# Performance work log

Hardware: AMD Instinct MI355X
Metric: run time of the kernel (lower is better)

## Reference

```python
import jax, jax.numpy as jnp
import numpy as np

D_MODEL, D_INNER, D_CONV, D_STATE, DT_RANK = 1024, 2048, 4, 16, 64
ALPHA, CHUNK = 0.1, 64


def setup_inputs() -> dict:
    key = jax.random.key(0)
    ks = jax.random.split(key, 10)
    B, T = 2, 2048
    s = lambda k, shape, scale: jax.random.normal(k, shape, jnp.float32) * scale
    return {
        "x": s(ks[0], (B, T, D_MODEL), 1.0),
        "norm1_w": jnp.ones((D_MODEL,), jnp.float32),
        "norm2_w": jnp.ones((D_MODEL,), jnp.float32),
        "in_proj_w": s(ks[1], (2 * D_INNER, D_MODEL), 0.02),
        "in_proj_b": jnp.zeros((2 * D_INNER,), jnp.float32),
        "conv_w": s(ks[2], (D_INNER, 1, D_CONV), 0.1),
        "conv_b": jnp.zeros((D_INNER,), jnp.float32),
        "x_proj_w": s(ks[3], (DT_RANK + 2 * D_STATE, D_INNER), 0.02),
        "dt_proj_w": s(ks[4], (D_INNER, DT_RANK), 0.02),
        "dt_proj_b": s(ks[5], (D_INNER,), 0.02),
        "A_log": jnp.log(jnp.broadcast_to(jnp.arange(1, D_STATE + 1, dtype=jnp.float32), (D_INNER, D_STATE))) + 0.0,
        "D_ssm": jnp.ones((D_INNER,), jnp.float32),
        "out_proj_w": s(ks[6], (D_MODEL, D_INNER), 0.02),
        "out_proj_b": jnp.zeros((D_MODEL,), jnp.float32),
        "proj_write_w": s(ks[7], (D_MODEL, D_MODEL), 0.02),
        "proj_read_w": s(ks[8], (D_MODEL, D_MODEL), 0.02),
        "decay": jnp.float32(4.6),
    }


def rmsnorm(x, w, eps=1e-5):
    return x * jax.lax.rsqrt(jnp.mean(x * x, axis=-1, keepdims=True) + eps) * w


def mamba_block(x, in_w, in_b, conv_w, conv_b, xp_w, dt_w, dt_b, A_log, D_ssm, out_w, out_b):
    # canonical (mamba-minimal) selective-SSM block
    B, T, _ = x.shape
    xz = x @ in_w.T + in_b                      # (B,T,2*d_inner)
    xm, res = jnp.split(xz, 2, axis=-1)
    # causal depthwise conv over time
    xc = jax.lax.conv_general_dilated(
        xm.transpose(0, 2, 1), conv_w, (1,), [(D_CONV - 1, 0)],
        dimension_numbers=("NCH", "OIH", "NCH"), feature_group_count=D_INNER)
    xm = jax.nn.silu(xc.transpose(0, 2, 1) + conv_b)
    x_dbl = xm @ xp_w.T                         # (B,T,dt_rank+2*d_state)
    delta = jax.nn.softplus(x_dbl[..., :DT_RANK] @ dt_w.T + dt_b)
    Bm = x_dbl[..., DT_RANK:DT_RANK + D_STATE]
    Cm = x_dbl[..., DT_RANK + D_STATE:]
    A = -jnp.exp(A_log)                          # (d_inner, d_state)

    def step(h, ins):
        d_t, B_t, C_t, u_t = ins                 # (B,di),(B,ds),(B,ds),(B,di)
        dA = jnp.exp(d_t[:, :, None] * A)
        h = h * dA + (d_t * u_t)[:, :, None] * B_t[:, None, :]
        y = jnp.einsum("bds,bs->bd", h, C_t)
        return h, y

    h0 = jnp.zeros((B, D_INNER, D_STATE), x.dtype)
    _, ys = jax.lax.scan(step, h0, (delta.transpose(1, 0, 2), Bm.transpose(1, 0, 2),
                                    Cm.transpose(1, 0, 2), xm.transpose(1, 0, 2)))
    y = ys.transpose(1, 0, 2) + xm * D_ssm
    y = y * jax.nn.silu(res)
    return y @ out_w.T + out_b


def memory_attend(out, w_write, w_read, decay):
    # chunked Hebbian write/read (RetNet-style chunked linear attention)
    B, T, D = out.shape
    C = CHUNK
    gamma = jax.nn.sigmoid(decay)
    log_gamma = jnp.log(gamma)
    v = out @ w_write.T
    wk = jnp.pad(out[:, :-1], ((0, 0), (1, 0), (0, 0)))
    rk = out
    n = T // C
    p = jnp.arange(C)
    diffs = jnp.clip(p[:, None] - 1 - p[None, :], 0, None).astype(out.dtype)
    causal = (p[:, None] > p[None, :]).astype(out.dtype)
    M = jnp.exp(diffs * log_gamma) * causal      # (C,C) intra-chunk decay mask
    g_in = gamma ** p                            # (C,)
    g_w = gamma ** (C - 1 - p)                   # (C,)

    chunked = lambda a: a.reshape(B, n, C, D).transpose(1, 0, 2, 3)  # (n,B,C,D)

    def step(W, ins):
        rk_c, wk_c, v_c = ins                    # each (B,C,D)
        inter = jnp.einsum("bde,bce->bcd", W, rk_c) * g_in[None, :, None]
        S = jnp.einsum("bcd,bkd->bck", rk_c, wk_c)
        intra = jnp.einsum("bck,bkd->bcd", S * M, v_c)
        W_new = (gamma ** C) * W + jnp.einsum("bcd,bce->bde", v_c * g_w[None, :, None], wk_c)
        return W_new, inter + intra

    W0 = jnp.zeros((B, D, D), out.dtype)
    _, reads = jax.lax.scan(step, W0, (chunked(rk), chunked(wk), chunked(v)))
    reads = reads.transpose(1, 0, 2, 3).reshape(B, T, D)
    return out + ALPHA * (reads @ w_read.T)


def reference(x, norm1_w, norm2_w, in_proj_w, in_proj_b, conv_w, conv_b, x_proj_w,
              dt_proj_w, dt_proj_b, A_log, D_ssm, out_proj_w, out_proj_b,
              proj_write_w, proj_read_w, decay):
    mb = lambda h: mamba_block(h, in_proj_w, in_proj_b, conv_w, conv_b, x_proj_w,
                               dt_proj_w, dt_proj_b, A_log, D_ssm, out_proj_w, out_proj_b)
    out1 = mb(rmsnorm(x, norm1_w))
    x1 = x + out1
    out2 = mb(rmsnorm(x1, norm2_w))   # tied weights: same params as mamba1
    out2 = memory_attend(out2, proj_write_w, proj_read_w, decay)
    return x1 + out2
```

## Files before the change

### kernel.cpp

```cpp
#include <hip/hip_runtime.h>
#include <hip/hip_bf16.h>
#include <math.h>

typedef __hip_bfloat16 bf16;
typedef __attribute__((ext_vector_type(4))) float f32x4;
typedef __attribute__((ext_vector_type(8))) short bf16x8;
typedef __attribute__((ext_vector_type(8))) unsigned short u16x8;

static __device__ __forceinline__ float b2f(bf16 v) { return __bfloat162float(v); }
static __device__ __forceinline__ float us2f(unsigned short u) {
  union { unsigned short s; bf16 h; } c; c.s = u; return __bfloat162float(c.h);
}
static __device__ __forceinline__ void  stv(float* p, float v) { *p = v; }
static __device__ __forceinline__ void  stv(bf16* p, float v) { *p = __float2bfloat16(v); }
static __device__ __forceinline__ float ldin(const void* p, size_t i, int f) {
  return f ? ((const float*)p)[i] : b2f(((const bf16*)p)[i]);
}
static __device__ __forceinline__ unsigned short f2b(float x) {
  bf16 h = __float2bfloat16(x);
  return *reinterpret_cast<unsigned short*>(&h);
}

static __device__ __forceinline__ void gl16(const unsigned short* g,
                                            void* ldsbase, int byteoff) {
  __builtin_amdgcn_global_load_lds(
      (const __attribute__((address_space(1))) unsigned int*)g,
      (__attribute__((address_space(3))) unsigned int*)((char*)ldsbase + byteoff),
      16, 0, 0);
}

constexpr int B_  = 2;
constexpr int T_  = 2048;
constexpr int DM  = 1024;
constexpr int DI  = 2048;
constexpr int DS  = 16;
constexpr int DTR = 64;
constexpr int ROWS = B_ * T_;
constexpr int SL  = 32;
constexpr int NSC = T_ / SL;
constexpr int KSP = 4;

__global__ void detect_k(const void* __restrict__ decay, int* __restrict__ flag) {
  flag[0] = (((const unsigned short*)decay)[0] == 0x4093) ? 0 : 1;
  flag[1] = 0;
}

__global__ void sentinel_k(void* __restrict__ out, float val, int n,
                           const int* __restrict__ df) {
  int f = *df;
  int i = blockIdx.x * 256 + threadIdx.x;
  if (i < n) {
    if (f) ((float*)out)[i] = val;
    else   ((bf16*)out)[i] = __float2bfloat16(val);
  }
}

__global__ void cvt1_k(const void* __restrict__ src, bf16* __restrict__ dst, int n,
                       const int* __restrict__ df) {
  int f = *df;
  int i = blockIdx.x * 256 + threadIdx.x;
  if (i < n) stv(&dst[i], ldin(src, i, f));
}

__global__ void rmsnorm_k(const void* __restrict__ xin, const void* __restrict__ w,
                          bf16* __restrict__ out, const int* __restrict__ df,
                          int xin_raw) {
  int f = *df;
  int fx = xin_raw ? f : 0;
  int row = blockIdx.x;
  int tid = threadIdx.x;
  float ss = 0.f;
  for (int d = tid; d < DM; d += 256) {
    float v = ldin(xin, (size_t)row * DM + d, fx);
    ss += v * v;
  }
  for (int o = 32; o > 0; o >>= 1) ss += __shfl_down(ss, o, 64);
  __shared__ float sred[4];
  int lane = tid & 63, wid = tid >> 6;
  if (lane == 0) sred[wid] = ss;
  __syncthreads();
  if (tid == 0) {
    float t = sred[0] + sred[1] + sred[2] + sred[3];
    sred[0] = 1.f / sqrtf(t / DM + 1e-5f);
  }
  __syncthreads();
  float rs = sred[0];
  for (int d = tid; d < DM; d += 256) {
    float v = ldin(xin, (size_t)row * DM + d, fx);
    stv(&out[(size_t)row * DM + d], v * rs * ldin(w, d, f));
  }
}

__global__ void transpose_k(const bf16* __restrict__ src, bf16* __restrict__ dst) {
  __shared__ unsigned short tile[64][65];
  int b = blockIdx.z;
  int t0 = blockIdx.x * 64, d0 = blockIdx.y * 64;
  int tid = threadIdx.x;
  int lt = tid & 63, lq = tid >> 6;
  const unsigned short* sp = (const unsigned short*)src;
  unsigned short* dp = (unsigned short*)dst;
#pragma unroll
  for (int i = 0; i < 16; i++) {
    int r = lq * 16 + i;
    tile[r][lt] = sp[((size_t)b * T_ + t0 + r) * DM + d0 + lt];
  }
  __syncthreads();
#pragma unroll
  for (int i = 0; i < 16; i++) {
    int r = lq * 16 + i;
    dp[((size_t)b * DM + d0 + r) * T_ + t0 + lt] = tile[lt][r];
  }
}

__global__ __launch_bounds__(512, 2)
void gemm256_k(const bf16* __restrict__ A, int lda,
               const void* __restrict__ B, int ldb,
               const void* __restrict__ bias,
               bf16* __restrict__ C, int ldc, int K,
               const int* __restrict__ df) {
  __shared__ alignas(16) unsigned char smem[65536];
  int f = *df;
  int m0 = blockIdx.y * 256, n0 = blockIdx.x * 256;
  int tid = threadIdx.x;
  int wave = tid >> 6, lane = tid & 63, quad = lane >> 4, l15 = lane & 15;
  int wrow = wave >> 2, wcol = wave & 3;
  const unsigned short* Ag = (const unsigned short*)A;
  const unsigned short* Bg = (const unsigned short*)B;
  f32x4 acc[8][4] = {};

  int r0 = tid >> 2;
  int kc = (((tid & 3) ^ ((r0 >> 1) & 3))) * 8;
  int xq = (quad ^ ((l15 >> 1) & 3)) * 16;

  auto stg = [&](int t, int isB, int dd) {
    const unsigned short* src = isB ? Bg : Ag;
    int ld = isB ? ldb : lda;
    int x0 = isB ? n0 : m0;
    int rbase = (isB ? 32768 : 0) + dd * 16384;
    int kk = t * 32;
    gl16(src + (size_t)(x0 + r0) * ld + kk + kc, smem, rbase + wave * 1024);
    gl16(src + (size_t)(x0 + r0 + 128) * ld + kk + kc, smem,
         rbase + 8192 + wave * 1024);
  };
  auto rdA = [&](int dd, int fr) {
    return *(const bf16x8*)(smem + dd * 16384 + wrow * 8192 + fr * 1024 +
                            l15 * 64 + xq);
  };
  auto rdB = [&](int dd, int fc) {
    return *(const bf16x8*)(smem + 32768 + dd * 16384 + wcol * 4096 +
                            fc * 1024 + l15 * 64 + xq);
  };

  int NT = K >> 5;
  if (f) {
    for (int t = 0; t < NT; ++t) {
      stg(t, 0, 0);
      {
        int r = tid >> 1, h = (tid & 1) * 16;
        const float* bp = (const float*)B + (size_t)(n0 + r) * ldb + t * 32 + h;
        float4 x0 = *(const float4*)bp,       x1 = *(const float4*)(bp + 4);
        float4 x2 = *(const float4*)(bp + 8), x3 = *(const float4*)(bp + 12);
        union { unsigned short s[8]; uint4 v; } p0, p1;
        p0.s[0]=f2b(x0.x); p0.s[1]=f2b(x0.y); p0.s[2]=f2b(x0.z); p0.s[3]=f2b(x0.w);
        p0.s[4]=f2b(x1.x); p0.s[5]=f2b(x1.y); p0.s[6]=f2b(x1.z); p0.s[7]=f2b(x1.w);
        p1.s[0]=f2b(x2.x); p1.s[1]=f2b(x2.y); p1.s[2]=f2b(x2.z); p1.s[3]=f2b(x2.w);
        p1.s[4]=f2b(x3.x); p1.s[5]=f2b(x3.y); p1.s[6]=f2b(x3.z); p1.s[7]=f2b(x3.w);
        int rx = (r >> 1) & 3;
        int c0 = (tid & 1) * 2;
        *(uint4*)(smem + 32768 + r * 64 + ((c0 ^ rx) * 16))       = p0.v;
        *(uint4*)(smem + 32768 + r * 64 + (((c0 + 1) ^ rx) * 16)) = p1.v;
      }
      __syncthreads();
      bf16x8 af[8], bv0, bv1, bv2, bv3;
#pragma unroll
      for (int fr = 0; fr < 8; fr++) af[fr] = rdA(0, fr);
      bv0 = rdB(0, 0); bv1 = rdB(0, 1); bv2 = rdB(0, 2); bv3 = rdB(0, 3);
#pragma unroll
      for (int fr = 0; fr < 8; fr++) {
        acc[fr][0] = __builtin_amdgcn_mfma_f32_16x16x32_bf16(af[fr], bv0, acc[fr][0], 0, 0, 0);
        acc[fr][1] = __builtin_amdgcn_mfma_f32_16x16x32_bf16(af[fr], bv1, acc[fr][1], 0, 0, 0);
        acc[fr][2] = __builtin_amdgcn_mfma_f32_16x16x32_bf16(af[fr], bv2, acc[fr][2], 0, 0, 0);
        acc[fr][3] = __builtin_amdgcn_mfma_f32_16x16x32_bf16(af[fr], bv3, acc[fr][3], 0, 0, 0);
      }
      __syncthreads();
    }
  } else {
    stg(0, 0, 0); stg(0, 1, 0);
    stg(1, 0, 1);
    asm volatile("s_waitcnt vmcnt(2)" ::: "memory");
    __builtin_amdgcn_sched_barrier(0);
    __builtin_amdgcn_s_barrier();
    for (int t = 0; t < NT; ++t) {
      int d = t & 1;
      bf16x8 af[8], bv0, bv1;
#pragma unroll
      for (int fr = 0; fr < 8; fr++) af[fr] = rdA(d, fr);
      bv0 = rdB(d, 0); bv1 = rdB(d, 1);
      if (t + 1 < NT) stg(t + 1, 1, d ^ 1);
      __builtin_amdgcn_s_barrier();
      asm volatile("s_waitcnt lgkmcnt(0)" ::: "memory");
      __builtin_amdgcn_sched_barrier(0);
      __builtin_amdgcn_s_setprio(1);
#pragma unroll
      for (int fr = 0; fr < 8; fr++) {
        acc[fr][0] = __builtin_amdgcn_mfma_f32_16x16x32_bf16(af[fr], bv0, acc[fr][0], 0, 0, 0);
        acc[fr][1] = __builtin_amdgcn_mfma_f32_16x16x32_bf16(af[fr], bv1, acc[fr][1], 0, 0, 0);
      }
      __builtin_amdgcn_s_setprio(0);
      __builtin_amdgcn_s_barrier();
      bf16x8 bv2, bv3;
      bv2 = rdB(d, 2); bv3 = rdB(d, 3);
      if (t + 2 < NT) stg(t + 2, 0, d);
      __builtin_amdgcn_s_barrier();
      asm volatile("s_waitcnt lgkmcnt(0)" ::: "memory");
      __builtin_amdgcn_sched_barrier(0);
      __builtin_amdgcn_s_setprio(1);
#pragma unroll
      for (int fr = 0; fr < 8; fr++) {
        acc[fr][2] = __builtin_amdgcn_mfma_f32_16x16x32_bf16(af[fr], bv2, acc[fr][2], 0, 0, 0);
        acc[fr][3] = __builtin_amdgcn_mfma_f32_16x16x32_bf16(af[fr], bv3, acc[fr][3], 0, 0, 0);
      }
      __builtin_amdgcn_s_setprio(0);
      if (t + 1 < NT) {
        if (t + 2 < NT)
          asm volatile("s_waitcnt vmcnt(2)" ::: "memory");
        else
          asm volatile("s_waitcnt vmcnt(0)" ::: "memory");
        __builtin_amdgcn_sched_barrier(0);
        __builtin_amdgcn_s_barrier();
      }
    }
  }

#pragma unroll
  for (int fr = 0; fr < 8; fr++) {
#pragma unroll
    for (int rr = 0; rr < 4; rr++) {
      int row = m0 + wrow * 128 + fr * 16 + quad * 4 + rr;
#pragma unroll
      for (int fc = 0; fc < 4; fc++) {
        int col = n0 + wcol * 64 + fc * 16 + l15;
        float v = acc[fr][fc][rr];
        if (bias) v += ldin(bias, col, f);
        C[(size_t)row * ldc + col] = __float2bfloat16(v);
      }
    }
  }
}

template <int MODE, int ACT, int MROWS>
__global__ void mgemm_k(const bf16* __restrict__ A, size_t sAz, int lda,
                        const void* __restrict__ B, size_t sBz, int ldb,
                        const void* __restrict__ bias,
                        bf16* __restrict__ C, size_t sCz, int ldc,
                        int M, int N, int K,
                        const void* __restrict__ dec, const int* __restrict__ df) {
  constexpr int FR = MROWS / 32;
  int by = (MODE == 2) ? ((int)gridDim.y - 1 - (int)blockIdx.y) : (int)blockIdx.y;
  int m0 = by * MROWS, n0 = blockIdx.x * 128;
  if (MODE == 1 && n0 > m0 + MROWS - 1) return;
  int f = *df;
  int bz = blockIdx.z;
  const bf16* Ab = A + (size_t)bz * sAz;
  const unsigned short* Bb16 =
      (const unsigned short*)B + (size_t)bz * sBz;
  bf16* Cb = C + (size_t)bz * sCz;
  int kmax = (MODE == 2) ? (m0 + MROWS) : K;
  __shared__ alignas(16) unsigned short As[2][MROWS][32];
  __shared__ alignas(16) unsigned short Bs[2][128][32];
  int tid = threadIdx.x;
  int wave = tid >> 6, lane = tid & 63, quad = lane >> 4, l15 = lane & 15;
  int wr = (wave >> 1) * (MROWS / 2), wc = (wave & 1) * 64;
  f32x4 acc[FR][4] = {};
  int lrow = lane >> 2;
  int lh = (((lane & 3) ^ ((lrow >> 1) & 3))) * 8;
  int xqs = (quad ^ ((l15 >> 1) & 3)) * 8;
  const unsigned short* Aus = (const unsigned short*)Ab;

  auto stage = [&](int buf, int k0) {
    if (MROWS == 128) {
#pragma unroll
      for (int q = 0; q < 2; q++) {
        int seg = wave * 2 + q;
        int rowa = seg * 16 + lrow;
        gl16(Aus + (size_t)(m0 + rowa) * lda + k0 + lh, &As[buf][0][0],
             seg * 1024);
      }
    } else {
      int rowa = wave * 16 + lrow;
      gl16(Aus + (size_t)(m0 + rowa) * lda + k0 + lh, &As[buf][0][0],
           wave * 1024);
    }
    if (MODE == 0 && f) {
      int r = tid >> 1, h = (tid & 1) * 16;
      const float* bp = (const float*)B + (size_t)(n0 + r) * ldb + k0 + h;
      float4 x0 = *(const float4*)bp,       x1 = *(const float4*)(bp + 4);
      float4 x2 = *(const float4*)(bp + 8), x3 = *(const float4*)(bp + 12);
      union { unsigned short s[8]; uint4 v; } p0, p1;
      p0.s[0]=f2b(x0.x); p0.s[1]=f2b(x0.y); p0.s[2]=f2b(x0.z); p0.s[3]=f2b(x0.w);
      p0.s[4]=f2b(x1.x); p0.s[5]=f2b(x1.y); p0.s[6]=f2b(x1.z); p0.s[7]=f2b(x1.w);
      p1.s[0]=f2b(x2.x); p1.s[1]=f2b(x2.y); p1.s[2]=f2b(x2.z); p1.s[3]=f2b(x2.w);
      p1.s[4]=f2b(x3.x); p1.s[5]=f2b(x3.y); p1.s[6]=f2b(x3.z); p1.s[7]=f2b(x3.w);
      int rx = (r >> 1) & 3;
      int c0 = (tid & 1) * 2;
      *(uint4*)&Bs[buf][r][(c0 ^ rx) * 8]       = p0.v;
      *(uint4*)&Bs[buf][r][((c0 + 1) ^ rx) * 8] = p1.v;
    } else {
#pragma unroll
      for (int q = 0; q < 2; q++) {
        int seg = wave * 2 + q;
        int rowb = seg * 16 + lrow;
        gl16(Bb16 + (size_t)(n0 + rowb) * ldb + k0 + lh, &Bs[buf][0][0],
             seg * 1024);
      }
    }
  };

  auto compute = [&](int buf) {
    bf16x8 af[FR], bfv[4];
#pragma unroll
    for (int i = 0; i < FR; i++)
      af[i] = *(const bf16x8*)&As[buf][wr + 16 * i + l15][xqs];
#pragma unroll
    for (int j = 0; j < 4; j++)
      bfv[j] = *(const bf16x8*)&Bs[buf][wc + 16 * j + l15][xqs];
#pragma unroll
    for (int i = 0; i < FR; i++)
#pragma unroll
      for (int j = 0; j < 4; j++)
        acc[i][j] = __builtin_amdgcn_mfma_f32_16x16x32_bf16(af[i], bfv[j],
                                                            acc[i][j], 0, 0, 0);
  };

  int nt = kmax >> 5;
  stage(0, 0);
  __syncthreads();
  int cur = 0;
  for (int t = 0; t < nt - 1; ++t) {
    stage(cur ^ 1, (t + 1) * 32);
    compute(cur);
    __syncthreads();
    cur ^= 1;
  }
  compute(cur);

  float lg = 0.f;
  if (MODE == 1) {
    float g = 1.f / (1.f + __expf(-ldin(dec, 0, f)));
    lg = __logf(g);
  }
#pragma unroll
  for (int i = 0; i < FR; i++) {
#pragma unroll
    for (int rr = 0; rr < 4; rr++) {
      int row = m0 + wr + 16 * i + quad * 4 + rr;
      if (MODE == 1 && n0 == 0 && wc == 0 && l15 == 0)
        Cb[(size_t)row * ldc] = __float2bfloat16(0.f);
#pragma unroll
      for (int j = 0; j < 4; j++) {
        int col = n0 + wc + 16 * j + l15;
        float v = acc[i][j][rr];
        if (MODE == 0) {
          if (bias) v += ldin(bias, col, f);
          if (ACT == 1) v = (v > 20.f) ? v : log1pf(__expf(v));
          Cb[(size_t)row * ldc + col] = __float2bfloat16(v);
        } else if (MODE == 1) {
          int colp = col + 1;
          int d_ = row - colp;
          v = (d_ > 0) ? v * __expf(lg * (float)(d_ - 1)) : 0.f;
          if (colp < N)
            Cb[(size_t)row * ldc + colp] = __float2bfloat16(v);
        } else {
          Cb[(size_t)row * ldc + col] = __float2bfloat16(v);
        }
      }
    }
  }
}

__global__ void conv_silu_k(const bf16* __restrict__ xz, const void* __restrict__ cw,
                            const void* __restrict__ cb, bf16* __restrict__ xm,
                            const int* __restrict__ df) {
  int f = *df;
  int i = blockIdx.x * 256 + threadIdx.x;
  int d8 = i & (DI / 8 - 1);
  int t = (i >> 8) & (T_ - 1);
  int b = i >> 19;
  int d0 = d8 * 8;
  const unsigned short* xzu =
      (const unsigned short*)xz + (size_t)b * T_ * 2 * DI + d0;

  float w[8][4], bias8[8];
  if (f) {
    const float* cwf = (const float*)cw + (size_t)d0 * 4;
#pragma unroll
    for (int j = 0; j < 8; j++) {
      float4 q = *(const float4*)(cwf + j * 4);
      w[j][0] = q.x; w[j][1] = q.y; w[j][2] = q.z; w[j][3] = q.w;
    }
    float4 b0 = *(const float4*)((const float*)cb + d0);
    float4 b1 = *(const float4*)((const float*)cb + d0 + 4);
    bias8[0] = b0.x; bias8[1] = b0.y; bias8[2] = b0.z; bias8[3] = b0.w;
    bias8[4] = b1.x; bias8[5] = b1.y; bias8[6] = b1.z; bias8[7] = b1.w;
  } else {
    const unsigned short* cwu = (const unsigned short*)cw + (size_t)d0 * 4;
#pragma unroll
    for (int jj = 0; jj < 4; jj++) {
      u16x8 q = *(const u16x8*)(cwu + jj * 8);
#pragma unroll
      for (int e = 0; e < 8; e++)
        w[(jj * 8 + e) >> 2][(jj * 8 + e) & 3] = us2f(q[e]);
    }
    u16x8 bb = *(const u16x8*)((const unsigned short*)cb + d0);
#pragma unroll
    for (int j = 0; j < 8; j++) bias8[j] = us2f(bb[j]);
  }

  float s[8];
#pragma unroll
  for (int j = 0; j < 8; j++) s[j] = bias8[j];

  if (t >= 3) {
    u16x8 v0 = *(const u16x8*)(xzu + (size_t)(t - 3) * 2 * DI);
    u16x8 v1 = *(const u16x8*)(xzu + (size_t)(t - 2) * 2 * DI);
    u16x8 v2 = *(const u16x8*)(xzu + (size_t)(t - 1) * 2 * DI);
    u16x8 v3 = *(const u16x8*)(xzu + (size_t)t * 2 * DI);
#pragma unroll
    for (int j = 0; j < 8; j++)
      s[j] += w[j][0] * us2f(v0[j]) + w[j][1] * us2f(v1[j]) +
              w[j][2] * us2f(v2[j]) + w[j][3] * us2f(v3[j]);
  } else {
#pragma unroll
    for (int k = 0; k < 4; k++) {
      int tt = t - 3 + k;
      if (tt >= 0) {
        u16x8 v = *(const u16x8*)(xzu + (size_t)tt * 2 * DI);
#pragma unroll
        for (int j = 0; j < 8; j++) s[j] += w[j][k] * us2f(v[j]);
      }
    }
  }
  union { unsigned short us[8]; u16x8 v; } o;
#pragma unroll
  for (int j = 0; j < 8; j++)
    o.us[j] = f2b(s[j] / (1.f + __expf(-s[j])));
  *(u16x8*)((unsigned short*)xm + (size_t)i * 8) = o.v;
}

__global__ void xproj_k(const bf16* __restrict__ xm, const void* __restrict__ xpw,
                        bf16* __restrict__ parts, const int* __restrict__ df) {
  int f = *df;
  int m0 = blockIdx.x * 128;
  int z = blockIdx.y;
  int kbase = z * (DI / KSP);
  __shared__ alignas(16) unsigned short As[2][128][32];
  __shared__ alignas(16) unsigned short Bs[2][96][32];
  int tid = threadIdx.x;
  int wave = tid >> 6, lane = tid & 63, quad = lane >> 4, l15 = lane & 15;
  int wr = wave * 32;
  f32x4 acc[2][6] = {};
  int lrow = lane >> 2;
  int lh = (((lane & 3) ^ ((lrow >> 1) & 3))) * 8;
  int xqs = (quad ^ ((l15 >> 1) & 3)) * 8;
  const unsigned short* Aus = (const unsigned short*)xm;
  const unsigned short* Bus = (const unsigned short*)xpw;

  auto stage = [&](int buf, int k0) {
#pragma unroll
    for (int q = 0; q < 2; q++) {
      int seg = wave * 2 + q;
      int rowa = seg * 16 + lrow;
      gl16(Aus + (size_t)(m0 + rowa) * DI + kbase + k0 + lh, &As[buf][0][0],
           seg * 1024);
    }
    if (f) {
      if (tid < 192) {
        int r2 = tid >> 1, h2 = (tid & 1) * 16;
        const float* bp = (const float*)xpw + (size_t)r2 * DI + kbase + k0 + h2;
        float4 x0 = *(const float4*)bp,       x1 = *(const float4*)(bp + 4);
        float4 x2 = *(const float4*)(bp + 8), x3 = *(const float4*)(bp + 12);
        union { unsigned short s[8]; uint4 v; } p0, p1;
        p0.s[0]=f2b(x0.x); p0.s[1]=f2b(x0.y); p0.s[2]=f2b(x0.z); p0.s[3]=f2b(x0.w);
        p0.s[4]=f2b(x1.x); p0.s[5]=f2b(x1.y); p0.s[6]=f2b(x1.z); p0.s[7]=f2b(x1.w);
        p1.s[0]=f2b(x2.x); p1.s[1]=f2b(x2.y); p1.s[2]=f2b(x2.z); p1.s[3]=f2b(x2.w);
        p1.s[4]=f2b(x3.x); p1.s[5]=f2b(x3.y); p1.s[6]=f2b(x3.z); p1.s[7]=f2b(x3.w);
        int rx = (r2 >> 1) & 3;
        int c0 = (tid & 1) * 2;
        *(uint4*)&Bs[buf][r2][(c0 ^ rx) * 8]       = p0.v;
        *(uint4*)&Bs[buf][r2][((c0 + 1) ^ rx) * 8] = p1.v;
      }
    } else if (wave < 3) {
#pragma unroll
      for (int q = 0; q < 2; q++) {
        int seg = wave * 2 + q;
        int rowb = seg * 16 + lrow;
        gl16(Bus + (size_t)rowb * DI + kbase + k0 + lh, &Bs[buf][0][0],
             seg * 1024);
      }
    }
  };

  auto compute = [&](int buf) {
    bf16x8 af[2], bfv[6];
#pragma unroll
    for (int i = 0; i < 2; i++)
      af[i] = *(const bf16x8*)&As[buf][wr + 16 * i + l15][xqs];
#pragma unroll
    for (int j = 0; j < 6; j++)
      bfv[j] = *(const bf16x8*)&Bs[buf][16 * j + l15][xqs];
#pragma unroll
    for (int i = 0; i < 2; i++)
#pragma unroll
      for (int j = 0; j < 6; j++)
        acc[i][j] = __builtin_amdgcn_mfma_f32_16x16x32_bf16(af[i], bfv[j],
                                                            acc[i][j], 0, 0, 0);
  };

  constexpr int NT = (DI / KSP) / 32;
  stage(0, 0);
  __syncthreads();
  int cur = 0;
  for (int t = 0; t < NT - 1; ++t) {
    stage(cur ^ 1, (t + 1) * 32);
    compute(cur);
    __syncthreads();
    cur ^= 1;
  }
  compute(cur);

  bf16* out = parts + (size_t)z * ROWS * 96;
#pragma unroll
  for (int i = 0; i < 2; i++)
#pragma unroll
    for (int rr = 0; rr < 4; rr++) {
      int row = m0 + wr + 16 * i + quad * 4 + rr;
#pragma unroll
      for (int j = 0; j < 6; j++) {
        int col = 16 * j + l15;
        out[(size_t)row * 96 + col] = __float2bfloat16(acc[i][j][rr]);
      }
    }
}

__global__ void reduce_xdbl_k(const bf16* __restrict__ parts, bf16* __restrict__ xdbl) {
  int i = blockIdx.x * 256 + threadIdx.x;
  if (i >= ROWS * 96) return;
  float s = 0.f;
#pragma unroll
  for (int z = 0; z < KSP; z++) s += b2f(parts[(size_t)z * ROWS * 96 + i]);
  stv(&xdbl[i], s);
}

__global__ void scan_p1_k(const bf16* __restrict__ delta, const bf16* __restrict__ xm,
                          const bf16* __restrict__ xdbl,
                          const void* __restrict__ alog,
                          bf16* __restrict__ F, float* __restrict__ S,
                          const int* __restrict__ df) {
  int f = *df;
  int idx = blockIdx.x * 256 + threadIdx.x;
  int d = idx & (DI - 1);
  int c = (idx >> 11) & (NSC - 1);
  int b = idx >> 17;
  float A[DS], hh[DS];
  bool fastA = true;
#pragma unroll
  for (int s = 0; s < DS; s++) {
    A[s] = -__expf(ldin(alog, d * DS + s, f));
    fastA = fastA && (fabsf(A[s] + (float)(s + 1)) < 1e-3f);
    hh[s] = 0.f;
  }
  int cs = c * SL;
  float ssum = 0.f;
  if (fastA) {
    for (int t = cs; t < cs + SL; t++) {
      size_t r = (size_t)b * T_ + t;
      float dlt = b2f(delta[r * DI + d]);
      float u = b2f(xm[r * DI + d]);
      ssum += dlt;
      float du = dlt * u;
      float q = __expf(-dlt);
      u16x8 t0 = *(const u16x8*)(xdbl + r * 96 + 64);
      u16x8 t1 = *(const u16x8*)(xdbl + r * 96 + 72);
      float e = 1.f;
#pragma unroll
      for (int s = 0; s < 8; s++) {
        e *= q; hh[s] = hh[s] * e + du * us2f(t0[s]);
      }
#pragma unroll
      for (int s = 0; s < 8; s++) {
        e *= q; hh[8 + s] = hh[8 + s] * e + du * us2f(t1[s]);
      }
    }
  } else {
    for (int t = cs; t < cs + SL; t++) {
      size_t r = (size_t)b * T_ + t;
      float dlt = b2f(delta[r * DI + d]);
      float u = b2f(xm[r * DI + d]);
      ssum += dlt;
      float du = dlt * u;
      u16x8 t0 = *(const u16x8*)(xdbl + r * 96 + 64);
      u16x8 t1 = *(const u16x8*)(xdbl + r * 96 + 72);
#pragma unroll
      for (int s = 0; s < 8; s++) {
        hh[s]     = hh[s]     * __expf(dlt * A[s])     + du * us2f(t0[s]);
        hh[8 + s] = hh[8 + s] * __expf(dlt * A[8 + s]) + du * us2f(t1[s]);
      }
    }
  }
#pragma unroll
  for (int s = 0; s < DS; s++) stv(&F[(size_t)idx * 16 + s], hh[s]);
  S[idx] = ssum;
}

__global__ void scan_p2_k(bf16* __restrict__ F, const float* __restrict__ S,
                          const void* __restrict__ alog, const int* __restrict__ df) {
  int f = *df;
  int idx = blockIdx.x * 256 + threadIdx.x;
  int s = idx & 15;
  int d = (idx >> 4) & (DI - 1);
  int b = idx >> 15;
  float As_ = -__expf(ldin(alog, d * DS + s, f));
  float H = 0.f;
  for (int c = 0; c < NSC; c++) {
    size_t base = (size_t)(b * NSC + c) * DI + d;
    float tmp = b2f(F[base * 16 + s]);
    stv(&F[base * 16 + s], H);
    H = __expf(As_ * S[base]) * H + tmp;
  }
}

__global__ void scan_p3_k(bf16* __restrict__ delta, const bf16* __restrict__ xm,
                          const bf16* __restrict__ xz, const bf16* __restrict__ xdbl,
                          const void* __restrict__ alog, const void* __restrict__ dssm,
                          const bf16* __restrict__ F, const int* __restrict__ df) {
  int f = *df;
  int idx = blockIdx.x * 256 + threadIdx.x;
  int d = idx & (DI - 1);
  int c = (idx >> 11) & (NSC - 1);
  int b = idx >> 17;
  float A[DS], hh[DS];
  bool fastA = true;
#pragma unroll
  for (int s = 0; s < DS; s++) {
    A[s] = -__expf(ldin(alog, d * DS + s, f));
    fastA = fastA && (fabsf(A[s] + (float)(s + 1)) < 1e-3f);
    hh[s] = b2f(F[(size_t)idx * 16 + s]);
  }
  float Dv = ldin(dssm, d, f);
  int cs = c * SL;
  if (fastA) {
    for (int t = cs; t < cs + SL; t++) {
      size_t r = (size_t)b * T_ + t;
      float dlt = b2f(delta[r * DI + d]);
      float u = b2f(xm[r * DI + d]);
      float du = dlt * u;
      float q = __expf(-dlt);
      u16x8 t0 = *(const u16x8*)(xdbl + r * 96 + 64);
      u16x8 t1 = *(const u16x8*)(xdbl + r * 96 + 72);
      u16x8 t2 = *(const u16x8*)(xdbl + r * 96 + 80);
      u16x8 t3 = *(const u16x8*)(xdbl + r * 96 + 88);
      float y = 0.f;
      float e = 1.f;
#pragma unroll
      for (int s = 0; s < 8; s++) {
        e *= q;
        hh[s] = hh[s] * e + du * us2f(t0[s]);
        y += hh[s] * us2f(t2[s]);
      }
#pragma unroll
      for (int s = 0; s < 8; s++) {
        e *= q;
        hh[8 + s] = hh[8 + s] * e + du * us2f(t1[s]);
        y += hh[8 + s] * us2f(t3[s]);
      }
      float res = b2f(xz[r * 2 * DI + DI + d]);
      y += u * Dv;
      y *= res / (1.f + __expf(-res));
      stv(&delta[r * DI + d], y);
    }
  } else {
    for (int t = cs; t < cs + SL; t++) {
      size_t r = (size_t)b * T_ + t;
      float dlt = b2f(delta[r * DI + d]);
      float u = b2f(xm[r * DI + d]);
      float du = dlt * u;
      u16x8 t0 = *(const u16x8*)(xdbl + r * 96 + 64);
      u16x8 t1 = *(const u16x8*)(xdbl + r * 96 + 72);
      u16x8 t2 = *(const u16x8*)(xdbl + r * 96 + 80);
      u16x8 t3 = *(const u16x8*)(xdbl + r * 96 + 88);
      float y = 0.f;
#pragma unroll
      for (int s = 0; s < 8; s++) {
        hh[s]     = hh[s]     * __expf(dlt * A[s])     + du * us2f(t0[s]);
        hh[8 + s] = hh[8 + s] * __expf(dlt * A[8 + s]) + du * us2f(t1[s]);
        y += hh[s] * us2f(t2[s]) + hh[8 + s] * us2f(t3[s]);
      }
      float res = b2f(xz[r * 2 * DI + DI + d]);
      y += u * Dv;
      y *= res / (1.f + __expf(-res));
      stv(&delta[r * DI + d], y);
    }
  }
}

__global__ void add_x1_k(const void* __restrict__ x, const bf16* __restrict__ o1,
                         bf16* __restrict__ x1, const int* __restrict__ df) {
  int f = *df;
  int i = blockIdx.x * 256 + threadIdx.x;
  if (i < ROWS * DM) stv(&x1[i], ldin(x, i, f) + b2f(o1[i]));
}

__global__ void final_k(const bf16* __restrict__ x1, const bf16* __restrict__ out2,
                        const bf16* __restrict__ rproj, void* __restrict__ out,
                        const int* __restrict__ df) {
  int f = *df;
  int i = blockIdx.x * 256 + threadIdx.x;
  if (i < ROWS * DM) {
    float v = b2f(x1[i]) + b2f(out2[i]) + 0.1f * b2f(rproj[i]);
    if (f) ((float*)out)[i] = v;
    else   stv(&((bf16*)out)[i], v);
  }
}

extern "C" void kernel_launch(void* const* d_in, const int* in_sizes, int n_in,
                              void* d_out, int out_size, void* d_ws, size_t ws_size,
                              hipStream_t stream) {
  (void)in_sizes; (void)n_in;
  const void* x    = d_in[0];
  const void* n1w  = d_in[1];
  const void* n2w  = d_in[2];
  const void* ipw  = d_in[3];
  const void* ipb  = d_in[4];
  const void* cw   = d_in[5];
  const void* cb   = d_in[6];
  const void* xpw  = d_in[7];
  const void* dtw  = d_in[8];
  const void* dtb  = d_in[9];
  const void* alog = d_in[10];
  const void* dssm = d_in[11];
  const void* opw  = d_in[12];
  const void* opb  = d_in[13];
  const void* pww  = d_in[14];
  const void* prw  = d_in[15];
  const void* dec  = d_in[16];

  char* base = (char*)d_ws;
  bf16*  xz    = (bf16*) (base + 0);
  bf16*  v     = (bf16*) (base + 0);
  bf16*  reads = (bf16*) (base + 8388608);
  bf16*  P     = (bf16*) (base + 16777216);
  bf16*  delta = (bf16*) (base + 33554432);
  bf16*  hnorm = delta;
  bf16*  rproj = (bf16*) (base + 33554432);
  bf16*  vt    = (bf16*) (base + 41943040);
  bf16*  xm    = (bf16*) (base + 50331648);
  bf16*  xdbl  = (bf16*) (base + 67108864);
  bf16*  parts = (bf16*) (base + 67895296);
  float* S     = (float*)(base + 67895296);
  bf16*  bout  = (bf16*) (base + 71041024);
  bf16*  F     = (bf16*) (base + 71041024);
  bf16*  x1    = (bf16*) (base + 79429632);
  int*   dflag = (int*)  (base + 87818240);
  bf16*  wbuf  = (bf16*) (base + 87818256);
  constexpr size_t WS_MIN = 87818248;
  constexpr int O_IPW = 0;
  constexpr int O_OPW = 4194304;
  constexpr int O_PWW = 6291456;
  constexpr int O_PRW = 7340032;
  constexpr int O_XPW = 8388608;
  constexpr int O_DTW = 8585216;
  constexpr int O_IPB = 8716288;
  constexpr int O_OPB = 8720384;
  constexpr int O_DTB = 8721408;
  constexpr int W_TOT = 8723456;
  constexpr size_t WS_BIG = 87818256 + (size_t)W_TOT * 2;

  detect_k<<<1, 1, 0, stream>>>(dec, dflag);
  if (ws_size < WS_MIN) {
    sentinel_k<<<(out_size + 255) / 256, 256, 0, stream>>>(
        d_out, (float)(ws_size >> 20), out_size, dflag);
    return;
  }

  const void *g_ipw = ipw, *g_ipb = ipb, *g_xpw = xpw, *g_dtw = dtw,
             *g_dtb = dtb, *g_opw = opw, *g_opb = opb, *g_pww = pww, *g_prw = prw;
  const int* wf = dflag;
  if (ws_size >= WS_BIG) {
    auto cvt = [&](const void* src, int off, int n) {
      cvt1_k<<<(n + 255) / 256, 256, 0, stream>>>(src, wbuf + off, n, dflag);
    };
    cvt(ipw, O_IPW, 4194304); cvt(opw, O_OPW, 2097152);
    cvt(pww, O_PWW, 1048576); cvt(prw, O_PRW, 1048576);
    cvt(xpw, O_XPW, 196608);  cvt(dtw, O_DTW, 131072);
    cvt(ipb, O_IPB, 4096);    cvt(opb, O_OPB, 1024);   cvt(dtb, O_DTB, 2048);
    g_ipw = wbuf + O_IPW; g_opw = wbuf + O_OPW; g_pww = wbuf + O_PWW;
    g_prw = wbuf + O_PRW; g_xpw = wbuf + O_XPW; g_dtw = wbuf + O_DTW;
    g_ipb = wbuf + O_IPB; g_opb = wbuf + O_OPB; g_dtb = wbuf + O_DTB;
    wf = dflag + 1;
  }

  auto mamba = [&](const void* xin, int xin_raw, const void* nw, bf16* outb) {
    rmsnorm_k<<<ROWS, 256, 0, stream>>>(xin, nw, hnorm, dflag, xin_raw);
    gemm256_k<<<dim3((2 * DI) / 256, ROWS / 256), 512, 0, stream>>>(
        hnorm, DM, g_ipw, DM, g_ipb, xz, 2 * DI, DM, wf);
    conv_silu_k<<<(ROWS * DI / 8) / 256, 256, 0, stream>>>(xz, cw, cb, xm, dflag);
    xproj_k<<<dim3(32, KSP), 256, 0, stream>>>(xm, g_xpw, parts, wf);
    reduce_xdbl_k<<<(ROWS * 96) / 256, 256, 0, stream>>>(parts, xdbl);
    mgemm_k<0, 1, 128><<<dim3(16, 32, 1), 256, 0, stream>>>(
        xdbl, 0, 96, g_dtw, 0, DTR, g_dtb, delta, 0, DI, ROWS, DI, DTR, dec, wf);
    scan_p1_k<<<B_ * NSC * DI / 256, 256, 0, stream>>>(delta, xm, xdbl, alog, F, S, dflag);
    scan_p2_k<<<B_ * DI * 16 / 256, 256, 0, stream>>>(F, S, alog, dflag);
    scan_p3_k<<<B_ * NSC * DI / 256, 256, 0, stream>>>(delta, xm, xz, xdbl, alog, dssm, F, dflag);
    mgemm_k<0, 0, 64><<<dim3(8, 64, 1), 256, 0, stream>>>(
        delta, 0, DI, g_opw, 0, DI, g_opb, outb, 0, DM, ROWS, DM, DI, dec, wf);
  };

  mamba(x, 1, n1w, bout);
  add_x1_k<<<(ROWS * DM) / 256, 256, 0, stream>>>(x, bout, x1, dflag);
  mamba(x1, 0, n2w, bout);

  mgemm_k<0, 0, 64><<<dim3(8, 64, 1), 256, 0, stream>>>(
      bout, 0, DM, g_pww, 0, DM, nullptr, v, 0, DM, ROWS, DM, DM, dec, wf);
  transpose_k<<<dim3(T_ / 64, DM / 64, B_), 256, 0, stream>>>(v, vt);
  mgemm_k<1, 0, 64><<<dim3(16, 32, B_), 256, 0, stream>>>(
      bout, (size_t)T_ * DM, DM, bout, (size_t)T_ * DM, DM, nullptr,
      P, (size_t)T_ * T_, T_, T_, T_, DM, dec, dflag);
  mgemm_k<2, 0, 64><<<dim3(8, 32, B_), 256, 0, stream>>>(
      P, (size_t)T_ * T_, T_, vt, (size_t)DM * T_, T_, nullptr,
      reads, (size_t)T_ * DM, DM, T_, DM, T_, dec, dflag);
  mgemm_k<0, 0, 64><<<dim3(8, 64, 1), 256, 0, stream>>>(
      reads, 0, DM, g_prw, 0, DM, nullptr, rproj, 0, DM, ROWS, DM, DM, dec, wf);
  final_k<<<(ROWS * DM) / 256, 256, 0, stream>>>(x1, bout, rproj, d_out, dflag);
}
```

Measured before the change: 815.5 us.

## Fuse residual adds into GEMM epilogues and double x_proj split-K

The first mamba block's out_proj GEMM now writes x1 directly by adding the input x in its epilogue, which removes the separate add_x1 kernel. The final proj_read GEMM writes the output as x1 + out2 + 0.1*reads_proj in its epilogue, which removes the rproj buffer round trip and final_k. The x_proj split-K factor goes from 4 to 8, with the extra partials stored in a second buffer, to raise parallelism in that small-grid GEMM. The cost is a larger reduce step that now reads eight partials.

Measured after the change: 806.7 us, median of 2. No clear change (-1.1%).

```diff
diff --git a/kernel.cpp b/kernel.cpp
--- a/kernel.cpp
+++ b/kernel.cpp
@@ -38,7 +38,7 @@
 constexpr int ROWS = B_ * T_;
 constexpr int SL  = 32;
 constexpr int NSC = T_ / SL;
-constexpr int KSP = 4;
+constexpr int KSP = 8;
 
 __global__ void detect_k(const void* __restrict__ decay, int* __restrict__ flag) {
   flag[0] = (((const unsigned short*)decay)[0] == 0x4093) ? 0 : 1;
@@ -248,18 +248,21 @@
   }
 }
 
-template <int MODE, int ACT, int MROWS>
+template <int MODE, int ACT, int MROWS, int EPI>
 __global__ void mgemm_k(const bf16* __restrict__ A, size_t sAz, int lda,
                         const void* __restrict__ B, size_t sBz, int ldb,
                         const void* __restrict__ bias,
                         bf16* __restrict__ C, size_t sCz, int ldc,
                         int M, int N, int K,
-                        const void* __restrict__ dec, const int* __restrict__ df) {
+                        const void* __restrict__ dec, const int* __restrict__ df,
+                        const void* __restrict__ eA, const bf16* __restrict__ eB,
+                        const int* __restrict__ efp) {
   constexpr int FR = MROWS / 32;
   int by = (MODE == 2) ? ((int)gridDim.y - 1 - (int)blockIdx.y) : (int)blockIdx.y;
   int m0 = by * MROWS, n0 = blockIdx.x * 128;
   if (MODE == 1 && n0 > m0 + MROWS - 1) return;
   int f = *df;
+  int ef = (EPI != 0) ? *efp : 0;
   int bz = blockIdx.z;
   const bf16* Ab = A + (size_t)bz * sAz;
   const unsigned short* Bb16 =
@@ -363,7 +366,16 @@
         if (MODE == 0) {
           if (bias) v += ldin(bias, col, f);
           if (ACT == 1) v = (v > 20.f) ? v : log1pf(__expf(v));
-          Cb[(size_t)row * ldc + col] = __float2bfloat16(v);
+          size_t oidx = (size_t)row * ldc + col;
+          if (EPI == 0) {
+            Cb[oidx] = __float2bfloat16(v);
+          } else if (EPI == 1) {
+            Cb[oidx] = __float2bfloat16(ldin(eA, oidx, ef) + v);
+          } else {
+            float o = b2f(((const bf16*)eA)[oidx]) + b2f(eB[oidx]) + 0.1f * v;
+            if (ef) ((float*)Cb)[oidx] = o;
+            else    Cb[oidx] = __float2bfloat16(o);
+          }
         } else if (MODE == 1) {
           int colp = col + 1;
           int d_ = row - colp;
@@ -448,7 +460,8 @@
 }
 
 __global__ void xproj_k(const bf16* __restrict__ xm, const void* __restrict__ xpw,
-                        bf16* __restrict__ parts, const int* __restrict__ df) {
+                        bf16* __restrict__ parts_lo, bf16* __restrict__ parts_hi,
+                        const int* __restrict__ df) {
   int f = *df;
   int m0 = blockIdx.x * 128;
   int z = blockIdx.y;
@@ -528,7 +541,8 @@
   }
   compute(cur);
 
-  bf16* out = parts + (size_t)z * ROWS * 96;
+  bf16* out = (z < 4) ? (parts_lo + (size_t)z * ROWS * 96)
+                      : (parts_hi + (size_t)(z - 4) * ROWS * 96);
 #pragma unroll
   for (int i = 0; i < 2; i++)
 #pragma unroll
@@ -542,12 +556,16 @@
     }
 }
 
-__global__ void reduce_xdbl_k(const bf16* __restrict__ parts, bf16* __restrict__ xdbl) {
+__global__ void reduce_xdbl_k(const bf16* __restrict__ parts_lo,
+                              const bf16* __restrict__ parts_hi,
+                              bf16* __restrict__ xdbl) {
   int i = blockIdx.x * 256 + threadIdx.x;
   if (i >= ROWS * 96) return;
   float s = 0.f;
 #pragma unroll
-  for (int z = 0; z < KSP; z++) s += b2f(parts[(size_t)z * ROWS * 96 + i]);
+  for (int z = 0; z < 4; z++) s += b2f(parts_lo[(size_t)z * ROWS * 96 + i]);
+#pragma unroll
+  for (int z = 0; z < 4; z++) s += b2f(parts_hi[(size_t)z * ROWS * 96 + i]);
   stv(&xdbl[i], s);
 }
 
@@ -751,7 +769,7 @@
   bf16*  P     = (bf16*) (base + 16777216);
   bf16*  delta = (bf16*) (base + 33554432);
   bf16*  hnorm = delta;
-  bf16*  rproj = (bf16*) (base + 33554432);
+  bf16*  phi   = (bf16*) (base + 33554432);
   bf16*  vt    = (bf16*) (base + 41943040);
   bf16*  xm    = (bf16*) (base + 50331648);
   bf16*  xdbl  = (bf16*) (base + 67108864);
@@ -799,36 +817,46 @@
     wf = dflag + 1;
   }
 
-  auto mamba = [&](const void* xin, int xin_raw, const void* nw, bf16* outb) {
+  auto mamba = [&](const void* xin, int xin_raw, const void* nw, bf16* outb,
+                   bool fuse_x1) {
     rmsnorm_k<<<ROWS, 256, 0, stream>>>(xin, nw, hnorm, dflag, xin_raw);
     gemm256_k<<<dim3((2 * DI) / 256, ROWS / 256), 512, 0, stream>>>(
         hnorm, DM, g_ipw, DM, g_ipb, xz, 2 * DI, DM, wf);
     conv_silu_k<<<(ROWS * DI / 8) / 256, 256, 0, stream>>>(xz, cw, cb, xm, dflag);
-    xproj_k<<<dim3(32, KSP), 256, 0, stream>>>(xm, g_xpw, parts, wf);
-    reduce_xdbl_k<<<(ROWS * 96) / 256, 256, 0, stream>>>(parts, xdbl);
-    mgemm_k<0, 1, 128><<<dim3(16, 32, 1), 256, 0, stream>>>(
-        xdbl, 0, 96, g_dtw, 0, DTR, g_dtb, delta, 0, DI, ROWS, DI, DTR, dec, wf);
+    xproj_k<<<dim3(32, KSP), 256, 0, stream>>>(xm, g_xpw, parts, phi, wf);
+    reduce_xdbl_k<<<(ROWS * 96) / 256, 256, 0, stream>>>(parts, phi, xdbl);
+    mgemm_k<0, 1, 128, 0><<<dim3(16, 32, 1), 256, 0, stream>>>(
+        xdbl, 0, 96, g_dtw, 0, DTR, g_dtb, delta, 0, DI, ROWS, DI, DTR, dec, wf,
+        nullptr, nullptr, nullptr);
     scan_p1_k<<<B_ * NSC * DI / 256, 256, 0, stream>>>(delta, xm, xdbl, alog, F, S, dflag);
     scan_p2_k<<<B_ * DI * 16 / 256, 256, 0, stream>>>(F, S, alog, dflag);
     scan_p3_k<<<B_ * NSC * DI / 256, 256, 0, stream>>>(delta, xm, xz, xdbl, alog, dssm, F, dflag);
-    mgemm_k<0, 0, 64><<<dim3(8, 64, 1), 256, 0, stream>>>(
-        delta, 0, DI, g_opw, 0, DI, g_opb, outb, 0, DM, ROWS, DM, DI, dec, wf);
+    if (fuse_x1)
+      mgemm_k<0, 0, 64, 1><<<dim3(8, 64, 1), 256, 0, stream>>>(
+          delta, 0, DI, g_opw, 0, DI, g_opb, x1, 0, DM, ROWS, DM, DI, dec, wf,
+          xin, nullptr, dflag);
+    else
+      mgemm_k<0, 0, 64, 0><<<dim3(8, 64, 1), 256, 0, stream>>>(
+          delta, 0, DI, g_opw, 0, DI, g_opb, outb, 0, DM, ROWS, DM, DI, dec, wf,
+          nullptr, nullptr, nullptr);
   };
 
-  mamba(x, 1, n1w, bout);
-  add_x1_k<<<(ROWS * DM) / 256, 256, 0, stream>>>(x, bout, x1, dflag);
-  mamba(x1, 0, n2w, bout);
-
-  mgemm_k<0, 0, 64><<<dim3(8, 64, 1), 256, 0, stream>>>(
-      bout, 0, DM, g_pww, 0, DM, nullptr, v, 0, DM, ROWS, DM, DM, dec, wf);
+  mamba(x, 1, n1w, bout, true);
+  mamba(x1, 0, n2w, bout, false);
+
+  mgemm_k<0, 0, 64, 0><<<dim3(8, 64, 1), 256, 0, stream>>>(
+      bout, 0, DM, g_pww, 0, DM, nullptr, v, 0, DM, ROWS, DM, DM, dec, wf,
+      nullptr, nullptr, nullptr);
   transpose_k<<<dim3(T_ / 64, DM / 64, B_), 256, 0, stream>>>(v, vt);
-  mgemm_k<1, 0, 64><<<dim3(16, 32, B_), 256, 0, stream>>>(
+  mgemm_k<1, 0, 64, 0><<<dim3(16, 32, B_), 256, 0, stream>>>(
       bout, (size_t)T_ * DM, DM, bout, (size_t)T_ * DM, DM, nullptr,
-      P, (size_t)T_ * T_, T_, T_, T_, DM, dec, dflag);
-  mgemm_k<2, 0, 64><<<dim3(8, 32, B_), 256, 0, stream>>>(
+      P, (size_t)T_ * T_, T_, T_, T_, DM, dec, dflag,
+      nullptr, nullptr, nullptr);
+  mgemm_k<2, 0, 64, 0><<<dim3(8, 32, B_), 256, 0, stream>>>(
       P, (size_t)T_ * T_, T_, vt, (size_t)DM * T_, T_, nullptr,
-      reads, (size_t)T_ * DM, DM, T_, DM, T_, dec, dflag);
-  mgemm_k<0, 0, 64><<<dim3(8, 64, 1), 256, 0, stream>>>(
-      reads, 0, DM, g_prw, 0, DM, nullptr, rproj, 0, DM, ROWS, DM, DM, dec, wf);
-  final_k<<<(ROWS * DM) / 256, 256, 0, stream>>>(x1, bout, rproj, d_out, dflag);
-}
+      reads, (size_t)T_ * DM, DM, T_, DM, T_, dec, dflag,
+      nullptr, nullptr, nullptr);
+  mgemm_k<0, 0, 64, 2><<<dim3(8, 64, 1), 256, 0, stream>>>(
+      reads, 0, DM, g_prw, 0, DM, nullptr, (bf16*)d_out, 0, DM, ROWS, DM, DM,
+      dec, wf, x1, bout, dflag);
+}
```
